# Performance work log

Measured on AMD Instinct MI355X. Metric: run time of the kernel, lower is better.

The kernel has to match this reference:

```python
import jax, jax.numpy as jnp
import numpy as np

KU, H, B, T = 512, 90, 32, 64
ALPHA = 0.5


def setup_inputs() -> dict:
    key = jax.random.key(0)
    ks = jax.random.split(key, 20)
    s = 0.1  # init scale ~ 1/sqrt(H)
    n = lambda k, shape: jax.random.normal(k, shape, jnp.float32) * s
    return {
        "questions": jax.random.randint(ks[0], (B, T), 0, KU),
        "answers": jax.random.randint(ks[1], (B, T), 0, 2 * KU),
        "response_emb": n(ks[2], (2 * KU, H)),
        "concept_emb": n(ks[3], (KU, H)),
        "nb_adj": (jax.random.uniform(ks[4], (KU, KU)) < 0.02).astype(jnp.float32),
        "succ_adj": (jax.random.uniform(ks[5], (KU, KU)) < 0.02).astype(jnp.float32),
        "Wi_self": n(ks[6], (H, 3 * H)), "Wh_self": n(ks[7], (H, 3 * H)),
        "bi_self": jnp.zeros((3 * H,), jnp.float32), "bh_self": jnp.zeros((3 * H,), jnp.float32),
        "Wi_rnn": n(ks[8], (H, 3 * H)), "Wh_rnn": n(ks[9], (H, 3 * H)),
        "bi_rnn": jnp.zeros((3 * H,), jnp.float32), "bh_rnn": jnp.zeros((3 * H,), jnp.float32),
        "W_sync": n(ks[10], (3 * H, H)), "b_sync": jnp.zeros((H,), jnp.float32),
        "W_prop": n(ks[11], (2 * H, H)), "b_prop": jnp.zeros((H,), jnp.float32),
        "W_agg": n(ks[12], (H, H)), "b_agg": jnp.zeros((H,), jnp.float32),
        "W_out": n(ks[13], (H, 1)), "b_out": jnp.zeros((1,), jnp.float32),
    }


def _gru(x, h, Wi, Wh, bi, bh):
    # standard GRU cell; works on [..., H]
    gi = x @ Wi + bi
    gh = h @ Wh + bh
    ir, iz, ig = jnp.split(gi, 3, axis=-1)
    hr, hz, hg = jnp.split(gh, 3, axis=-1)
    r = jax.nn.sigmoid(ir + hr)
    z = jax.nn.sigmoid(iz + hz)
    g = jnp.tanh(ig + r * hg)
    return (1.0 - z) * g + z * h


def reference(questions, answers, response_emb, concept_emb, nb_adj, succ_adj,
              Wi_self, Wh_self, bi_self, bh_self, Wi_rnn, Wh_rnn, bi_rnn, bh_rnn,
              W_sync, b_sync, W_prop, b_prop, W_agg, b_agg, W_out, b_out):
    batch = questions.shape[0]
    ku, hid = concept_emb.shape
    states0 = jnp.zeros((batch, ku, hid), jnp.float32)
    ce = jnp.broadcast_to(concept_emb[None], (batch, ku, hid))  # [B,K,H]
    bidx = jnp.arange(batch)

    def step(states, qa):
        q, a = qa  # [B], [B]
        self_state = states[bidx, q]                               # [B,H] gather
        next_self = _gru(response_emb[a], self_state, Wi_self, Wh_self, bi_self, bh_self)
        self_mask = jax.nn.one_hot(q, ku, dtype=states.dtype)[..., None]   # [B,K,1]
        nb_mask = nb_adj[q][..., None]                                      # [B,K,1]
        # sync: concat(states, broadcast next_self, concept embeds) -> MLP -> neighbor mask
        sync_diff = jnp.concatenate(
            [states, jnp.broadcast_to(next_self[:, None], (batch, ku, hid)), ce], axis=-1)
        sync_inf = nb_mask * jax.nn.relu(sync_diff @ W_sync + b_sync)       # [B,K,H]
        reflec = jnp.sum(sync_inf, axis=1, keepdims=True)                   # [B,1,H]
        sync_inf = sync_inf + self_mask * reflec
        # prop: (delta self state, concept emb of q) -> MLP -> successor mask
        prop_diff = jnp.concatenate([next_self - self_state, concept_emb[q]], axis=-1)  # [B,2H]
        prop_inf = jax.nn.relu(prop_diff @ W_prop + b_prop)                 # [B,H]
        prop_inf = succ_adj[q][..., None] * prop_inf[:, None]               # [B,K,H]
        inf = jax.nn.relu((ALPHA * sync_inf + (1.0 - ALPHA) * prop_inf) @ W_agg + b_agg)
        new_states = _gru(inf, states, Wi_rnn, Wh_rnn, bi_rnn, bh_rnn)      # [B,K,H]
        out = jax.nn.sigmoid(jnp.squeeze(new_states @ W_out + b_out, -1))   # [B,K]
        return new_states, out

    states, outputs = jax.lax.scan(step, states0, (questions.T, answers.T))
    return outputs, states  # outputs: [T,B,K], states: [B,K,H]
```

## Files before the change

kernel.cpp:

```cpp
#include <hip/hip_runtime.h>

#define KU 512
#define NB 32
#define NT 64
#define TIL 64
#define SLOTS 16
#define NBMAX 40

#define N_PONG   (KU * NB * 90)
#define OFF_CEB  (N_PONG)
#define OFF_GI0  (OFF_CEB + KU * 90)
#define OFF_WHTF (OFF_GI0 + 288)
#define OFF_SYF  (OFF_WHTF + 13824)
#define OFF_AGF  (OFF_SYF + 4608)
#define OFF_WIF  (OFF_AGF + 4608)
#define OFF_WISF (OFF_WIF + 13056)
#define OFF_WHSF (OFF_WISF + 13056)
#define OFF_SYMF (OFF_WHSF + 13056)
#define OFF_WPRF (OFF_SYMF + 4608)

typedef short bf16x8 __attribute__((ext_vector_type(8)));
typedef float f32x4 __attribute__((ext_vector_type(4)));

__device__ __forceinline__ float sigf(float x) { return 1.0f / (1.0f + __expf(-x)); }
__device__ __forceinline__ float tanhf_(float x) {
    float e = __expf(2.0f * x);
    return 1.0f - 2.0f / (e + 1.0f);
}
__device__ __forceinline__ unsigned short f2bf(float f) {
    union { float f; unsigned u; } v; v.f = f;
    unsigned r = v.u + 0x7FFFu + ((v.u >> 16) & 1u);
    return (unsigned short)(r >> 16);
}
__device__ __forceinline__ bf16x8 cvt8(const float* p) {
    const float4 a0 = *(const float4*)p;
    const float4 a1 = *(const float4*)(p + 4);
    union { bf16x8 v; unsigned short u[8]; } fr;
    fr.u[0] = f2bf(a0.x); fr.u[1] = f2bf(a0.y); fr.u[2] = f2bf(a0.z); fr.u[3] = f2bf(a0.w);
    fr.u[4] = f2bf(a1.x); fr.u[5] = f2bf(a1.y); fr.u[6] = f2bf(a1.z); fr.u[7] = f2bf(a1.w);
    return fr.v;
}
__device__ __forceinline__ f32x4 mm3(const bf16x8* af, const unsigned short* bp) {
    f32x4 d = f32x4{0.f, 0.f, 0.f, 0.f};
    d = __builtin_amdgcn_mfma_f32_16x16x32_bf16(af[0], *(const bf16x8*)(bp), d, 0, 0, 0);
    d = __builtin_amdgcn_mfma_f32_16x16x32_bf16(af[1], *(const bf16x8*)(bp + 512), d, 0, 0, 0);
    d = __builtin_amdgcn_mfma_f32_16x16x32_bf16(af[2], *(const bf16x8*)(bp + 1024), d, 0, 0, 0);
    return d;
}

__global__ void skt_prep(const float* __restrict__ concept_emb, const float* __restrict__ W_sync,
                         const float* __restrict__ b_sync, const float* __restrict__ Wi_rnn,
                         const float* __restrict__ Wh_rnn, const float* __restrict__ Wi_self,
                         const float* __restrict__ Wh_self, const float* __restrict__ W_prop,
                         const float* __restrict__ bi_rnn, const float* __restrict__ b_agg,
                         const float* __restrict__ W_agg, float* __restrict__ ws) {
    const int blk = blockIdx.x, tid = threadIdx.x;
    if (blk < 128) {
        for (int rr = 0; rr < 4; ++rr) {
            const int k = blk * 4 + rr;
            if (tid < 90) {
                float acc = b_sync[tid];
                for (int kk = 0; kk < 90; ++kk)
                    acc += concept_emb[k * 90 + kk] * W_sync[(180 + kk) * 90 + tid];
                ws[OFF_CEB + k * 90 + tid] = acc;
            }
        }
    } else if (blk < 131) {
        const int g = blk - 128;
        unsigned short* p = (unsigned short*)(ws + OFF_WHTF);
        for (int idx = tid; idx < 9216; idx += 256) {
            const int i = idx & 7, lane = (idx >> 3) & 63;
            const int rest = idx >> 9, kk = rest % 3, nb = rest / 3;
            const int n = nb * 16 + (lane & 15);
            const int k = kk * 32 + ((lane >> 4) << 3) + i;
            p[(size_t)g * 9216 + idx] = f2bf((n < 90 && k < 90) ? Wh_rnn[k * 270 + g * 90 + n] : 0.f);
        }
    } else if (blk == 131) {
        for (int c = tid; c < 272; c += 256) {
            float acc = 0.f;
            if (c < 270) {
                acc = bi_rnn[c];
                for (int kk = 0; kk < 90; ++kk)
                    acc += fmaxf(b_agg[kk], 0.f) * Wi_rnn[kk * 270 + c];
            }
            ws[OFF_GI0 + c] = acc;
        }
    } else if (blk == 132) {
        unsigned short* p = (unsigned short*)(ws + OFF_SYF);
        for (int idx = tid; idx < 9216; idx += 256) {
            const int i = idx & 7, lane = (idx >> 3) & 63;
            const int rest = idx >> 9, kk = rest % 3, nt = rest / 3;
            const int n = nt * 16 + (lane & 15);
            const int k = kk * 32 + ((lane >> 4) << 3) + i;
            p[idx] = f2bf((n < 90 && k < 90) ? W_sync[k * 90 + n] : 0.f);
        }
    } else if (blk == 133) {
        unsigned short* p = (unsigned short*)(ws + OFF_AGF);
        for (int idx = tid; idx < 9216; idx += 256) {
            const int i = idx & 7, lane = (idx >> 3) & 63;
            const int rest = idx >> 9, kk = rest % 3, nt = rest / 3;
            const int n = nt * 16 + (lane & 15);
            const int k = kk * 32 + ((lane >> 4) << 3) + i;
            p[idx] = f2bf((n < 90 && k < 90) ? W_agg[k * 90 + n] : 0.f);
        }
    } else if (blk < 136) {
        unsigned short* p = (unsigned short*)(ws + OFF_WIF);
        const int i0 = (blk - 134) * 13056, i1 = i0 + 13056;
        for (int idx = i0 + tid; idx < i1; idx += 256) {
            const int i = idx & 7, lane = (idx >> 3) & 63;
            const int rest = idx >> 9, kk = rest % 3, nt = rest / 3;
            const int n = nt * 16 + (lane & 15);
            const int k = kk * 32 + ((lane >> 4) << 3) + i;
            p[idx] = f2bf((n < 270 && k < 90) ? Wi_rnn[k * 270 + n] : 0.f);
        }
    } else if (blk < 138) {
        unsigned short* p = (unsigned short*)(ws + OFF_WISF);
        const int i0 = (blk - 136) * 13056, i1 = i0 + 13056;
        for (int idx = i0 + tid; idx < i1; idx += 256) {
            const int i = idx & 7, lane = (idx >> 3) & 63;
            const int rest = idx >> 9, kk = rest % 3, nt = rest / 3;
            const int n = nt * 16 + (lane & 15);
            const int k = kk * 32 + ((lane >> 4) << 3) + i;
            p[idx] = f2bf((n < 270 && k < 90) ? Wi_self[k * 270 + n] : 0.f);
        }
    } else if (blk < 140) {
        unsigned short* p = (unsigned short*)(ws + OFF_WHSF);
        const int i0 = (blk - 138) * 13056, i1 = i0 + 13056;
        for (int idx = i0 + tid; idx < i1; idx += 256) {
            const int i = idx & 7, lane = (idx >> 3) & 63;
            const int rest = idx >> 9, kk = rest % 3, nt = rest / 3;
            const int n = nt * 16 + (lane & 15);
            const int k = kk * 32 + ((lane >> 4) << 3) + i;
            p[idx] = f2bf((n < 270 && k < 90) ? Wh_self[k * 270 + n] : 0.f);
        }
    } else if (blk == 140) {
        unsigned short* p = (unsigned short*)(ws + OFF_SYMF);
        for (int idx = tid; idx < 9216; idx += 256) {
            const int i = idx & 7, lane = (idx >> 3) & 63;
            const int rest = idx >> 9, kk = rest % 3, nt = rest / 3;
            const int n = nt * 16 + (lane & 15);
            const int k = kk * 32 + ((lane >> 4) << 3) + i;
            p[idx] = f2bf((n < 90 && k < 90) ? W_sync[(90 + k) * 90 + n] : 0.f);
        }
    } else {
        unsigned short* p = (unsigned short*)(ws + OFF_WPRF);
        for (int idx = tid; idx < 18432; idx += 256) {
            const int i = idx & 7, lane = (idx >> 3) & 63;
            const int rest = idx >> 9, kk = rest % 6, nt = rest / 6;
            const int n = nt * 16 + (lane & 15);
            const int k = kk * 32 + ((lane >> 4) << 3) + i;
            p[idx] = f2bf((n < 90 && k < 180) ? W_prop[k * 90 + n] : 0.f);
        }
    }
}

__global__ __launch_bounds__(512, 1) void skt_step(
    const int* __restrict__ qs, const int* __restrict__ as_,
    const float* __restrict__ response_emb, const float* __restrict__ concept_emb,
    const float* __restrict__ nb_adj, const float* __restrict__ succ_adj,
    const float* __restrict__ bi_self, const float* __restrict__ bh_self,
    const float* __restrict__ bi_rnn, const float* __restrict__ bh_rnn,
    const float* __restrict__ b_agg, const float* __restrict__ b_prop,
    const float* __restrict__ W_out, const float* __restrict__ b_out,
    float* __restrict__ ws, const float* __restrict__ stIn, float* __restrict__ stOut,
    float* __restrict__ out, int t) {
    __shared__ alignas(16) float hR[TIL * 100];
    __shared__ alignas(16) float hnb[NBMAX * 96];
    __shared__ alignas(16) float rfd[NBMAX * 92];
    __shared__ alignas(16) float giL[SLOTS * 273];
    __shared__ alignas(16) float actb[SLOTS * 96], infb[SLOTS * 96];
    __shared__ alignas(16) float giA[272], ghA[272];
    __shared__ alignas(16) float gi0L[273], biL[273], bhL[272];
    __shared__ alignas(16) float re[96], ssv[96], ceq[96];
    __shared__ alignas(16) float nsvW[6][96], xpW[6][192];
    __shared__ alignas(16) float nsyL[96], pvL[96], baggL[96];
    __shared__ float nbw[NBMAX];
    __shared__ int nblist[NBMAX];
    __shared__ float nbvL[TIL], svL[TIL];
    __shared__ int rowslotS[TIL], listS[TIL];
    __shared__ int nactS, nnbS;

    const int tid = threadIdx.x;
    const int bb = blockIdx.x >> 3;
    const int k0 = (blockIdx.x & 7) * TIL;
    const int q = qs[bb * NT + t];
    const int a = as_[bb * NT + t];
    const bool owner = (q >= k0 && q < k0 + TIL);
    const bool havePrev = (t > 0);

    const int w8 = tid >> 6, lane = tid & 63;
    const int lr = lane & 15, lh = lane >> 4;
    const int rt = w8 & 3, cg = w8 >> 2;
    const bf16x8 z8 = {0, 0, 0, 0, 0, 0, 0, 0};

    const unsigned short* whtF = (const unsigned short*)(ws + OFF_WHTF);
    const unsigned short* syF = (const unsigned short*)(ws + OFF_SYF);
    const unsigned short* agF = (const unsigned short*)(ws + OFF_AGF);
    const unsigned short* wiF = (const unsigned short*)(ws + OFF_WIF);
    const unsigned short* wisF = (const unsigned short*)(ws + OFF_WISF);
    const unsigned short* whsF = (const unsigned short*)(ws + OFF_WHSF);
    const unsigned short* symF = (const unsigned short*)(ws + OFF_SYMF);
    const unsigned short* wprF = (const unsigned short*)(ws + OFF_WPRF);

    if (tid < 384) {
        for (int idx = tid; idx < TIL * 50; idx += 384) {
            const int row = idx / 50, c2 = idx - row * 50;
            float2 v = make_float2(0.f, 0.f);
            if (c2 < 45 && havePrev)
                v = ((const float2*)(stIn + ((size_t)(bb * KU + k0 + row)) * 90))[c2];
            *(float2*)&hR[row * 100 + 2 * c2] = v;
        }
    } else if (tid < 448) {
        const int l = tid - 384;
        const int kg = k0 + l;
        const float nv = nb_adj[(size_t)q * KU + kg];
        const float sv = succ_adj[(size_t)q * KU + kg];
        nbvL[l] = nv; svL[l] = sv;
        const bool act = (nv != 0.f) || (sv != 0.f) || (kg == q);
        const unsigned long long mb = __ballot(act);
        const int rank = (int)__popcll(mb & ((1ull << l) - 1ull));
        rowslotS[l] = act ? rank : -1;
        if (act) listS[rank] = l;
        if (l == 0) nactS = (int)__popcll(mb);
    } else {
        const int l = tid - 448;
        int base = 0;
        for (int ch = 0; ch < 8; ++ch) {
            const int kp = ch * 64 + l;
            const float nv = nb_adj[(size_t)q * KU + kp];
            const unsigned long long mb = __ballot(nv != 0.f);
            const int idx = base + (int)__popcll(mb & ((1ull << l) - 1ull));
            if (nv != 0.f && idx < NBMAX) { nblist[idx] = kp; nbw[idx] = nv; }
            base += (int)__popcll(mb);
        }
        if (l == 0) nnbS = (base < NBMAX) ? base : NBMAX;
    }
    for (int j = tid; j < 270; j += 512) {
        if (j < 90) re[j] = response_emb[(size_t)a * 90 + j];
        else if (j < 180) ssv[j - 90] = havePrev ? stIn[((size_t)(bb * KU + q)) * 90 + (j - 90)] : 0.f;
        else ceq[j - 180] = concept_emb[(size_t)q * 90 + (j - 180)];
    }
    for (int c = tid; c < 273; c += 512) {
        gi0L[c] = (c < 272) ? ws[OFF_GI0 + c] : 0.f;
        biL[c] = (c < 270) ? bi_rnn[c] : 0.f;
        if (c < 272) bhL[c] = (c < 270) ? bh_rnn[c] : 0.f;
    }
    if (tid < 96) {
        baggL[tid] = (tid < 90) ? b_agg[tid] : 0.f;
        if (tid >= 90) { re[tid] = 0.f; ssv[tid] = 0.f; ceq[tid] = 0.f; }
    } else if (tid < 132) {
        nsvW[(tid - 96) / 6][90 + (tid - 96) % 6] = 0.f;
    } else if (tid < 204) {
        xpW[(tid - 132) / 12][180 + (tid - 132) % 12] = 0.f;
    }
    for (int j2 = tid; j2 < SLOTS * 6 * 2; j2 += 512) {
        const int half = j2 >= SLOTS * 6;
        const int jj = half ? j2 - SLOTS * 6 : j2;
        (half ? infb : actb)[(jj / 6) * 96 + 90 + (jj % 6)] = 0.f;
    }
    if (havePrev) {
        const int row = tid >> 3, j = tid & 7;
        const float* sp = stIn + ((size_t)(bb * KU + k0 + row)) * 90;
        float p = 0.f;
#pragma unroll
        for (int mm = 0; mm < 12; ++mm) {
            const int m = j * 12 + mm;
            if (m < 90) p += sp[m] * W_out[m];
        }
#pragma unroll
        for (int o = 1; o < 8; o <<= 1) p += __shfl_xor(p, o);
        if (j == 0)
            out[(size_t)(t - 1) * NB * KU + (size_t)bb * KU + k0 + row] = sigf(p + b_out[0]);
    }
    __syncthreads();

    if (owner) {
        const int nnb = nnbS;
        for (int i = tid; i < nnb * 48; i += 512) {
            const int j = i / 48, c2 = i - j * 48;
            float2 v = make_float2(0.f, 0.f);
            if (c2 < 45 && havePrev)
                v = ((const float2*)(stIn + ((size_t)(bb * KU + nblist[j])) * 90))[c2];
            *(float2*)&hnb[j * 96 + 2 * c2] = v;
        }
    }
    {
        bf16x8 af[3];
#pragma unroll
        for (int kk = 0; kk < 3; ++kk)
            af[kk] = (lr == 0) ? cvt8(&re[kk * 32 + lh * 8])
                   : ((lr == 1) ? cvt8(&ssv[kk * 32 + lh * 8]) : z8);
        for (int nt = w8; nt < 17; nt += 8) {
            const f32x4 dwi = mm3(af, wisF + (size_t)nt * 1536 + lane * 8);
            const f32x4 dwh = mm3(af, whsF + (size_t)nt * 1536 + lane * 8);
            if (lh == 0) {
                const int c = nt * 16 + lr;
                if (c < 270) { giA[c] = bi_self[c] + dwi[0]; ghA[c] = bh_self[c] + dwh[1]; }
            }
        }
    }
    f32x4 acc[3][3];
#pragma unroll
    for (int g = 0; g < 3; ++g)
#pragma unroll
        for (int ct = 0; ct < 3; ++ct) acc[g][ct] = f32x4{0.f, 0.f, 0.f, 0.f};
    {
        bf16x8 afr[3];
        const float* ar = &hR[(rt * 16 + lr) * 100];
#pragma unroll
        for (int kk = 0; kk < 3; ++kk) afr[kk] = cvt8(ar + kk * 32 + lh * 8);
#pragma unroll
        for (int g = 0; g < 3; ++g) {
#pragma unroll
            for (int ct = 0; ct < 3; ++ct) {
                const int nb = cg * 3 + ct;
                const unsigned short* bp = whtF + (size_t)(g * 6 + nb) * 1536 + lane * 8;
                acc[g][ct] = __builtin_amdgcn_mfma_f32_16x16x32_bf16(afr[0], *(const bf16x8*)(bp), acc[g][ct], 0, 0, 0);
                acc[g][ct] = __builtin_amdgcn_mfma_f32_16x16x32_bf16(afr[1], *(const bf16x8*)(bp + 512), acc[g][ct], 0, 0, 0);
                acc[g][ct] = __builtin_amdgcn_mfma_f32_16x16x32_bf16(afr[2], *(const bf16x8*)(bp + 1024), acc[g][ct], 0, 0, 0);
            }
        }
    }
    __syncthreads();

    const int m6 = w8 * 16 + lr;
    if (w8 < 6) {
        {
            const int l1 = lane, l2 = lane + 64;
            if (l1 < 90) {
                const float r = sigf(giA[l1] + ghA[l1]);
                const float z = sigf(giA[90 + l1] + ghA[90 + l1]);
                const float g = tanhf_(giA[180 + l1] + r * ghA[180 + l1]);
                const float ns = (1.f - z) * g + z * ssv[l1];
                nsvW[w8][l1] = ns;
                xpW[w8][l1] = ns - ssv[l1];
                xpW[w8][90 + l1] = ceq[l1];
            }
            if (l2 < 90) {
                const float r = sigf(giA[l2] + ghA[l2]);
                const float z = sigf(giA[90 + l2] + ghA[90 + l2]);
                const float g = tanhf_(giA[180 + l2] + r * ghA[180 + l2]);
                const float ns = (1.f - z) * g + z * ssv[l2];
                nsvW[w8][l2] = ns;
                xpW[w8][l2] = ns - ssv[l2];
                xpW[w8][90 + l2] = ceq[l2];
            }
        }
        {
            bf16x8 af[3];
#pragma unroll
            for (int kk = 0; kk < 3; ++kk)
                af[kk] = (lr == 0) ? cvt8(&nsvW[w8][kk * 32 + lh * 8]) : z8;
            const f32x4 d = mm3(af, symF + (size_t)w8 * 1536 + lane * 8);
            if (lh == 0) nsyL[m6] = (m6 < 90) ? d[0] : 0.f;
        }
        {
            f32x4 d = f32x4{0.f, 0.f, 0.f, 0.f};
            const unsigned short* bp = wprF + (size_t)w8 * 3072 + lane * 8;
#pragma unroll
            for (int kk = 0; kk < 6; ++kk) {
                const bf16x8 av = (lr == 0) ? cvt8(&xpW[w8][kk * 32 + lh * 8]) : z8;
                d = __builtin_amdgcn_mfma_f32_16x16x32_bf16(av, *(const bf16x8*)(bp + kk * 512), d, 0, 0, 0);
            }
            if (lh == 0) pvL[m6] = (m6 < 90) ? fmaxf(b_prop[m6] + d[0], 0.f) : 0.f;
        }
    } else if (owner) {
        const int nnb = nnbS;
        const int pairs = ((nnb + 15) >> 4) * 6;
        for (int p = w8 - 6; p < pairs; p += 2) {
            const int mt = p / 6, nt = p - mt * 6;
            bf16x8 af[3];
            const int jrow = mt * 16 + lr;
            if (jrow < nnb) {
                const float* rp = &hnb[jrow * 96];
#pragma unroll
                for (int kk = 0; kk < 3; ++kk) af[kk] = cvt8(rp + kk * 32 + lh * 8);
            } else { af[0] = z8; af[1] = z8; af[2] = z8; }
            const f32x4 d = mm3(af, syF + (size_t)nt * 1536 + lane * 8);
#pragma unroll
            for (int r4 = 0; r4 < 4; ++r4) {
                const int j = mt * 16 + lh * 4 + r4;
                const int m = nt * 16 + lr;
                if (j < nnb && m < 90)
                    rfd[j * 92 + m] = d[r4] + ws[OFF_CEB + (size_t)nblist[j] * 90 + m];
            }
        }
    }
    __syncthreads();

    const int nact = nactS;
    const int npass0 = (nact + SLOTS - 1) / SLOTS;
    const int npass = (npass0 > 0) ? npass0 : 1;
    for (int pass = 0; pass < npass; ++pass) {
        const int e0p = pass * SLOTS;
        int e1p = e0p + SLOTS; if (e1p > nact) e1p = nact;
        const int na = e1p - e0p;

        if (na > 0 && w8 < 6) {
            const int nt = w8;
            bf16x8 af[3];
            if (lr < na) {
                const float* rp = &hR[listS[e0p + lr] * 100];
#pragma unroll
                for (int kk = 0; kk < 3; ++kk) af[kk] = cvt8(rp + kk * 32 + lh * 8);
            } else { af[0] = z8; af[1] = z8; af[2] = z8; }
            const f32x4 d = mm3(af, syF + (size_t)nt * 1536 + lane * 8);
            const int m = nt * 16 + lr;
            if (m < 90) {
#pragma unroll
                for (int r4 = 0; r4 < 4; ++r4) {
                    const int slot = lh * 4 + r4;
                    if (slot >= na) continue;
                    const int r = listS[e0p + slot];
                    const float nv = nbvL[r], sv = svL[r];
                    float s = 0.f;
                    if (nv != 0.f)
                        s = nv * fmaxf(nsyL[m] + ws[OFF_CEB + (size_t)(k0 + r) * 90 + m] + d[r4], 0.f);
                    if (k0 + r == q) {
                        const int nnb = nnbS;
                        const float nm = nsyL[m];
                        for (int j = 0; j < nnb; ++j)
                            s += nbw[j] * fmaxf(nm + rfd[j * 92 + m], 0.f);
                    }
                    actb[slot * 96 + m] = 0.5f * s + 0.5f * sv * pvL[m];
                }
            }
        }
        __syncthreads();

        if (na > 0 && w8 < 6) {
            const int nt = w8;
            bf16x8 af[3];
            if (lr < na) {
                const float* rp = &actb[lr * 96];
#pragma unroll
                for (int kk = 0; kk < 3; ++kk) af[kk] = cvt8(rp + kk * 32 + lh * 8);
            } else { af[0] = z8; af[1] = z8; af[2] = z8; }
            const f32x4 d = mm3(af, agF + (size_t)nt * 1536 + lane * 8);
            const int m = nt * 16 + lr;
            if (m < 90) {
#pragma unroll
                for (int r4 = 0; r4 < 4; ++r4) {
                    const int slot = lh * 4 + r4;
                    if (slot < na) infb[slot * 96 + m] = fmaxf(baggL[m] + d[r4], 0.f);
                }
            }
        }
        __syncthreads();

        if (na > 0) {
            bf16x8 af[3];
            if (lr < na) {
                const float* rp = &infb[lr * 96];
#pragma unroll
                for (int kk = 0; kk < 3; ++kk) af[kk] = cvt8(rp + kk * 32 + lh * 8);
            } else { af[0] = z8; af[1] = z8; af[2] = z8; }
            for (int nt = w8; nt < 17; nt += 8) {
                const f32x4 d = mm3(af, wiF + (size_t)nt * 1536 + lane * 8);
                const int c = nt * 16 + lr;
                if (c < 270) {
#pragma unroll
                    for (int r4 = 0; r4 < 4; ++r4) {
                        const int slot = lh * 4 + r4;
                        if (slot < na) giL[slot * 273 + c] = biL[c] + d[r4];
                    }
                }
            }
        }
        __syncthreads();

#pragma unroll
        for (int ct = 0; ct < 3; ++ct) {
            const int m = cg * 48 + ct * 16 + lr;
            if (m < 90) {
                const float bhr = bhL[m], bhz = bhL[90 + m], bhg = bhL[180 + m];
#pragma unroll
                for (int r4 = 0; r4 < 4; ++r4) {
                    const int row = rt * 16 + 4 * lh + r4;
                    const int sraw = rowslotS[row];
                    const bool mine = (sraw < 0) ? (pass == 0) : (sraw >= e0p && sraw < e1p);
                    if (!mine) continue;
                    const float* gs = (sraw < 0) ? gi0L : &giL[(sraw - e0p) * 273];
                    const float rg = sigf(gs[m] + acc[0][ct][r4] + bhr);
                    const float zg = sigf(gs[90 + m] + acc[1][ct][r4] + bhz);
                    const float gg = tanhf_(gs[180 + m] + rg * (acc[2][ct][r4] + bhg));
                    const float hold = hR[row * 100 + m];
                    const float hn = (1.f - zg) * gg + zg * hold;
                    hR[row * 100 + m] = hn;
                    stOut[((size_t)(bb * KU + k0 + row)) * 90 + m] = hn;
                }
            }
        }
        if (pass + 1 < npass) __syncthreads();
    }
}

__global__ __launch_bounds__(512, 1) void skt_final(
    const float* __restrict__ stFinal, const float* __restrict__ W_out,
    const float* __restrict__ b_out, float* __restrict__ out) {
    const int tid = threadIdx.x;
    const int bb = blockIdx.x >> 3;
    const int k0 = (blockIdx.x & 7) * TIL;
    const int row = tid >> 3, j = tid & 7;
    const float* sp = stFinal + ((size_t)(bb * KU + k0 + row)) * 90;
    float p = 0.f;
#pragma unroll
    for (int mm = 0; mm < 12; ++mm) {
        const int m = j * 12 + mm;
        if (m < 90) p += sp[m] * W_out[m];
    }
#pragma unroll
    for (int o = 1; o < 8; o <<= 1) p += __shfl_xor(p, o);
    if (j == 0)
        out[(size_t)(NT - 1) * NB * KU + (size_t)bb * KU + k0 + row] = sigf(p + b_out[0]);
}

extern "C" void kernel_launch(void* const* d_in, const int* in_sizes, int n_in,
                              void* d_out, int out_size, void* d_ws, size_t ws_size,
                              hipStream_t stream) {
    const int* questions = (const int*)d_in[0];
    const int* answers = (const int*)d_in[1];
    const float* response_emb = (const float*)d_in[2];
    const float* concept_emb = (const float*)d_in[3];
    const float* nb_adj = (const float*)d_in[4];
    const float* succ_adj = (const float*)d_in[5];
    const float* Wi_self = (const float*)d_in[6];
    const float* Wh_self = (const float*)d_in[7];
    const float* bi_self = (const float*)d_in[8];
    const float* bh_self = (const float*)d_in[9];
    const float* Wi_rnn = (const float*)d_in[10];
    const float* Wh_rnn = (const float*)d_in[11];
    const float* bi_rnn = (const float*)d_in[12];
    const float* bh_rnn = (const float*)d_in[13];
    const float* W_sync = (const float*)d_in[14];
    const float* b_sync = (const float*)d_in[15];
    const float* W_prop = (const float*)d_in[16];
    const float* b_prop = (const float*)d_in[17];
    const float* W_agg = (const float*)d_in[18];
    const float* b_agg = (const float*)d_in[19];
    const float* W_out = (const float*)d_in[20];
    const float* b_out = (const float*)d_in[21];

    float* out = (float*)d_out;
    float* stFinal = out + (size_t)NT * NB * KU;
    float* ws = (float*)d_ws;

    skt_prep<<<142, 256, 0, stream>>>(concept_emb, W_sync, b_sync, Wi_rnn, Wh_rnn,
                                      Wi_self, Wh_self, W_prop, bi_rnn, b_agg, W_agg, ws);
    for (int t = 0; t < NT; ++t) {
        const float* sin = (t & 1) ? ws : stFinal;
        float* sout = (t & 1) ? stFinal : ws;
        skt_step<<<NB * 8, 512, 0, stream>>>(
            questions, answers, response_emb, concept_emb, nb_adj, succ_adj,
            bi_self, bh_self, bi_rnn, bh_rnn, b_agg, b_prop, W_out, b_out,
            ws, sin, sout, out, t);
    }
    skt_final<<<NB * 8, 512, 0, stream>>>(stFinal, W_out, b_out, out);
}
```

Baseline: 1.477 ms.

## Process active rows per wave with wave-level sync instead of block barriers

Restructures the sync, aggregation and GRU-input matmul stages so that each wave handles one active row end to end. Every wave runs all column tiles with MFMA for its row and needs only a wave-local LDS wait between stages, rather than splitting column tiles across waves and using __syncthreads. This removes two block-wide barriers per pass. In exchange, each MFMA carries a single useful row (the A fragment is that row replicated), so matrix work per row grows sharply and each wave runs a longer serial chain of MFMAs.

```diff
diff --git a/kernel.cpp b/kernel.cpp
--- a/kernel.cpp
+++ b/kernel.cpp
@@ -47,6 +47,7 @@
     d = __builtin_amdgcn_mfma_f32_16x16x32_bf16(af[2], *(const bf16x8*)(bp + 1024), d, 0, 0, 0);
     return d;
 }
+#define WAVE_SYNC() { asm volatile("s_waitcnt lgkmcnt(0)" ::: "memory"); __builtin_amdgcn_sched_barrier(0); }
 
 __global__ void skt_prep(const float* __restrict__ concept_emb, const float* __restrict__ W_sync,
                          const float* __restrict__ b_sync, const float* __restrict__ Wi_rnn,
@@ -396,73 +397,70 @@
         int e1p = e0p + SLOTS; if (e1p > nact) e1p = nact;
         const int na = e1p - e0p;
 
-        if (na > 0 && w8 < 6) {
-            const int nt = w8;
-            bf16x8 af[3];
-            if (lr < na) {
-                const float* rp = &hR[listS[e0p + lr] * 100];
+        for (int s = w8; s < na; s += 8) {
+            const int r = listS[e0p + s];
+            const float nv = nbvL[r], sv = svL[r];
+            const bool isq = (k0 + r == q);
+
+            {
+                bf16x8 af[3];
+                const float* rp = &hR[r * 100];
 #pragma unroll
                 for (int kk = 0; kk < 3; ++kk) af[kk] = cvt8(rp + kk * 32 + lh * 8);
-            } else { af[0] = z8; af[1] = z8; af[2] = z8; }
-            const f32x4 d = mm3(af, syF + (size_t)nt * 1536 + lane * 8);
-            const int m = nt * 16 + lr;
-            if (m < 90) {
-#pragma unroll
-                for (int r4 = 0; r4 < 4; ++r4) {
-                    const int slot = lh * 4 + r4;
-                    if (slot >= na) continue;
-                    const int r = listS[e0p + slot];
-                    const float nv = nbvL[r], sv = svL[r];
-                    float s = 0.f;
-                    if (nv != 0.f)
-                        s = nv * fmaxf(nsyL[m] + ws[OFF_CEB + (size_t)(k0 + r) * 90 + m] + d[r4], 0.f);
-                    if (k0 + r == q) {
-                        const int nnb = nnbS;
-                        const float nm = nsyL[m];
-                        for (int j = 0; j < nnb; ++j)
-                            s += nbw[j] * fmaxf(nm + rfd[j * 92 + m], 0.f);
+                float dv[6];
+#pragma unroll
+                for (int nt = 0; nt < 6; ++nt)
+                    dv[nt] = mm3(af, syF + (size_t)nt * 1536 + lane * 8)[0];
+                if (lh == 0) {
+#pragma unroll
+                    for (int nt = 0; nt < 6; ++nt) {
+                        const int m = nt * 16 + lr;
+                        if (m < 90) {
+                            float sval = 0.f;
+                            if (nv != 0.f)
+                                sval = nv * fmaxf(nsyL[m] + ws[OFF_CEB + (size_t)(k0 + r) * 90 + m] + dv[nt], 0.f);
+                            if (isq) {
+                                const int nnb = nnbS;
+                                const float nm = nsyL[m];
+                                for (int j = 0; j < nnb; ++j)
+                                    sval += nbw[j] * fmaxf(nm + rfd[j * 92 + m], 0.f);
+                            }
+                            actb[s * 96 + m] = 0.5f * sval + 0.5f * sv * pvL[m];
+                        }
                     }
-                    actb[slot * 96 + m] = 0.5f * s + 0.5f * sv * pvL[m];
                 }
             }
-        }
-        __syncthreads();
-
-        if (na > 0 && w8 < 6) {
-            const int nt = w8;
-            bf16x8 af[3];
-            if (lr < na) {
-                const float* rp = &actb[lr * 96];
+            WAVE_SYNC();
+
+            {
+                bf16x8 af[3];
+                const float* rp = &actb[s * 96];
 #pragma unroll
                 for (int kk = 0; kk < 3; ++kk) af[kk] = cvt8(rp + kk * 32 + lh * 8);
-            } else { af[0] = z8; af[1] = z8; af[2] = z8; }
-            const f32x4 d = mm3(af, agF + (size_t)nt * 1536 + lane * 8);
-            const int m = nt * 16 + lr;
-            if (m < 90) {
-#pragma unroll
-                for (int r4 = 0; r4 < 4; ++r4) {
-                    const int slot = lh * 4 + r4;
-                    if (slot < na) infb[slot * 96 + m] = fmaxf(baggL[m] + d[r4], 0.f);
+                float dv[6];
+#pragma unroll
+                for (int nt = 0; nt < 6; ++nt)
+                    dv[nt] = mm3(af, agF + (size_t)nt * 1536 + lane * 8)[0];
+                if (lh == 0) {
+#pragma unroll
+                    for (int nt = 0; nt < 6; ++nt) {
+                        const int m = nt * 16 + lr;
+                        if (m < 90) infb[s * 96 + m] = fmaxf(baggL[m] + dv[nt], 0.f);
+                    }
                 }
             }
-        }
-        __syncthreads();
-
-        if (na > 0) {
-            bf16x8 af[3];
-            if (lr < na) {
-                const float* rp = &infb[lr * 96];
+            WAVE_SYNC();
+
+            {
+                bf16x8 af[3];
+                const float* rp = &infb[s * 96];
 #pragma unroll
                 for (int kk = 0; kk < 3; ++kk) af[kk] = cvt8(rp + kk * 32 + lh * 8);
-            } else { af[0] = z8; af[1] = z8; af[2] = z8; }
-            for (int nt = w8; nt < 17; nt += 8) {
-                const f32x4 d = mm3(af, wiF + (size_t)nt * 1536 + lane * 8);
-                const int c = nt * 16 + lr;
-                if (c < 270) {
-#pragma unroll
-                    for (int r4 = 0; r4 < 4; ++r4) {
-                        const int slot = lh * 4 + r4;
-                        if (slot < na) giL[slot * 273 + c] = biL[c] + d[r4];
+                for (int nt = 0; nt < 17; ++nt) {
+                    const float d0 = mm3(af, wiF + (size_t)nt * 1536 + lane * 8)[0];
+                    if (lh == 0) {
+                        const int c = nt * 16 + lr;
+                        if (c < 270) giL[s * 273 + c] = biL[c] + d0;
                     }
                 }
             }
```

New measurement: 3.665 ms. +148.1%, slower.
